# Kernel optimization log

Hardware: AMD Instinct MI355X
Metric: run time of the kernel (lower is better)

## Reference

```python
import jax, jax.numpy as jnp
import numpy as np
from jax import ops

N, E, F_IN, H, M, KC, B, C_OUT = 100000, 1600000, 128, 128, 150000, 60000, 64, 10
BN_EPS = 1e-5

def setup_inputs() -> dict:
    key = jax.random.key(0)
    ks = jax.random.split(key, 16)
    s = 0.05
    x = jax.random.normal(ks[0], (N, F_IN), jnp.float32)
    edge_index = jax.random.randint(ks[1], (2, E), 0, N)
    weights = jax.random.uniform(ks[2], (E,), jnp.float32)
    # sorted batch vector covering all B graphs
    batch = (jnp.arange(N) * B) // N
    # cover assignments: every cluster gets at least one node (arange prefix)
    cover_nodes = jax.random.randint(ks[3], (M,), 0, N)
    cover_clusters = jnp.concatenate([jnp.arange(KC), jax.random.randint(ks[4], (M - KC,), 0, KC)])
    cluster_batch = (jnp.arange(KC) * B) // KC
    out_dim = 4 * H  # 2 * num_layers * hidden, readout=True
    return {
        'x': x, 'edge_index': edge_index, 'weights': weights, 'batch': batch,
        'cover_nodes': cover_nodes, 'cover_clusters': cover_clusters, 'cluster_batch': cluster_batch,
        'W_in': jax.random.normal(ks[5], (F_IN, H), jnp.float32) * s,
        'b_in': jnp.zeros((H,), jnp.float32),
        'W_blk': jax.random.normal(ks[6], (2 * H, H), jnp.float32) * s,
        'b_blk': jnp.zeros((H,), jnp.float32),
        'bn_gamma': jnp.ones((out_dim,), jnp.float32),
        'bn_beta': jnp.zeros((out_dim,), jnp.float32),
        'bn_mean': jnp.zeros((out_dim,), jnp.float32),
        'bn_var': jnp.ones((out_dim,), jnp.float32),
        'W1': jax.random.normal(ks[7], (out_dim, H), jnp.float32) * s,
        'b1': jnp.zeros((H,), jnp.float32),
        'W2': jax.random.normal(ks[8], (H, C_OUT), jnp.float32) * s,
        'b2': jnp.zeros((C_OUT,), jnp.float32),
    }

def _gcn(x, src, dst, w, n, W, b):
    # PyG GCNConv: out = D^-1/2 (A + I) D^-1/2 (x W) + b, weighted degrees incl. self loop of 1
    deg = ops.segment_sum(w, dst, num_segments=n) + 1.0
    dinv = jax.lax.rsqrt(deg)
    xw = x @ W
    msg = (w * dinv[src] * dinv[dst])[:, None] * xw[src]          # [E,H]
    agg = ops.segment_sum(msg, dst, num_segments=n) + (dinv * dinv)[:, None] * xw
    return agg + b

def reference(x, edge_index, weights, batch, cover_nodes, cover_clusters, cluster_batch,
              W_in, b_in, W_blk, b_blk, bn_gamma, bn_beta, bn_mean, bn_var, W1, b1, W2, b2):
    src, dst = edge_index[0], edge_index[1]

    # conv_in + relu
    h = jax.nn.relu(_gcn(x, src, dst, weights, N, W_in, b_in))     # [N,H]

    counts = ops.segment_sum(jnp.ones((N,), jnp.float32), batch, num_segments=B)
    xs = [ops.segment_sum(h, batch, num_segments=B),               # global_add_pool
          ops.segment_max(h, batch, num_segments=B)]               # global_max_pool

    # --- pool_graphs: cover_pool_node (add & max) ---
    x_add = ops.segment_sum(h[cover_nodes], cover_clusters, num_segments=KC)
    x_max = ops.segment_max(h[cover_nodes], cover_clusters, num_segments=KC)
    xp = jnp.concatenate([x_add, x_max], axis=1)                   # [KC, 2H]

    # --- pooled GCN, matrix-free A' = C^T A C (cover_pool_edge, pool='add') ---
    def aprime(z):  # z: [KC, d]
        zn = ops.segment_sum(z[cover_clusters], cover_nodes, num_segments=N)   # C z
        ye = ops.segment_sum(weights[:, None] * zn[src], dst, num_segments=N)  # A (C z)
        return ops.segment_sum(ye[cover_nodes], cover_clusters, num_segments=KC)  # C^T ...

    degp = aprime(jnp.ones((KC, 1), jnp.float32))[:, 0] + 1.0      # weighted degree of A'+I
    dinv = jax.lax.rsqrt(degp)
    xw = xp @ W_blk                                                # [KC,H]
    xws = dinv[:, None] * xw
    hp = jax.nn.relu(dinv[:, None] * (aprime(xws) + xws) + b_blk)  # [KC,H]

    ccounts = ops.segment_sum(jnp.ones((KC,), jnp.float32), cluster_batch, num_segments=B)
    xs.append(ops.segment_sum(hp, cluster_batch, num_segments=B) / ccounts[:, None])  # mean pool
    xs.append(ops.segment_max(hp, cluster_batch, num_segments=B))

    z = jnp.concatenate(xs, axis=1)                                # [B, 4H]
    z = (z - bn_mean) * jax.lax.rsqrt(bn_var + BN_EPS) * bn_gamma + bn_beta  # BN (eval)
    z = jax.nn.relu(z @ W1 + b1)                                   # dropout=identity (eval)
    z = z @ W2 + b2
    return jax.nn.softmax(z, axis=-1)
```

## Files before the change

### kernel.cpp

```cpp
#include <hip/hip_runtime.h>


#define H 128
#define TILE_AGG 2048
#define GRID_AGG 784

typedef __attribute__((ext_vector_type(4))) float f32x4;
typedef __attribute__((ext_vector_type(8))) short bf16x8;

__device__ __forceinline__ void atomAddF(float* p, float v) {
    unsafeAtomicAdd(p, v);
}
__device__ __forceinline__ void atomMaxPos(float* p, float v) {
    atomicMax(reinterpret_cast<int*>(p), __float_as_int(v));
}

__device__ __forceinline__ unsigned int bfr(float f) {
    unsigned int u = __float_as_uint(f);
    return (u + 0x7fffu + ((u >> 16) & 1u)) >> 16;
}
__device__ __forceinline__ unsigned int pk2(float lo, float hi) {
    return bfr(lo) | (bfr(hi) << 16);
}
__device__ __forceinline__ float unlo(unsigned int v) { return __uint_as_float(v << 16); }
__device__ __forceinline__ float unhi(unsigned int v) { return __uint_as_float(v & 0xffff0000u); }

__global__ void count_pairs(const int* __restrict__ a, const int* __restrict__ b,
                            int* __restrict__ ca, int* __restrict__ cb, int M) {
    int i = blockIdx.x * blockDim.x + threadIdx.x;
    if (i < M) {
        atomicAdd(&ca[__builtin_nontemporal_load(a + i)], 1);
        atomicAdd(&cb[__builtin_nontemporal_load(b + i)], 1);
    }
}

__global__ __launch_bounds__(256) void scan_partial(const int* __restrict__ c,
                                                    int* __restrict__ part, int m) {
    __shared__ int red[4];
    int base = blockIdx.x * 1024, t = threadIdx.x;
    int s = 0;
    for (int j = t; j < 1024; j += 256) { int i = base + j; if (i < m) s += c[i]; }
    for (int o = 32; o; o >>= 1) s += __shfl_down(s, o, 64);
    if ((t & 63) == 0) red[t >> 6] = s;
    __syncthreads();
    if (t == 0) part[blockIdx.x] = red[0] + red[1] + red[2] + red[3];
}
__global__ void scan_spine(int* part, int G) {
    if (threadIdx.x == 0) {
        int acc = 0;
        for (int i = 0; i < G; ++i) { int v = part[i]; part[i] = acc; acc += v; }
    }
}
__global__ __launch_bounds__(256) void scan_apply(int* __restrict__ c,
                                                  const int* __restrict__ part, int m) {
    __shared__ int wsum[4];
    int base = blockIdx.x * 1024, t = threadIdx.x;
    int i0 = base + t * 4;
    int v0 = 0, v1 = 0, v2 = 0, v3 = 0;
    if (i0     < m) v0 = c[i0];
    if (i0 + 1 < m) v1 = c[i0 + 1];
    if (i0 + 2 < m) v2 = c[i0 + 2];
    if (i0 + 3 < m) v3 = c[i0 + 3];
    int ts = v0 + v1 + v2 + v3;
    int lane = t & 63, w = t >> 6;
    int sc = ts;
    for (int o = 1; o < 64; o <<= 1) { int u = __shfl_up(sc, o, 64); if (lane >= o) sc += u; }
    if (lane == 63) wsum[w] = sc;
    __syncthreads();
    int off = part[blockIdx.x];
    for (int k = 0; k < w; ++k) off += wsum[k];
    int ex = off + sc - ts;
    if (i0     < m) c[i0]     = ex;
    if (i0 + 1 < m) c[i0 + 1] = ex + v0;
    if (i0 + 2 < m) c[i0 + 2] = ex + v0 + v1;
    if (i0 + 3 < m) c[i0 + 3] = ex + v0 + v1 + v2;
}

__global__ void fill_pairs(const int* __restrict__ key, const int* __restrict__ val,
                           int* __restrict__ offs, int* __restrict__ slots, int M) {
    int i = blockIdx.x * blockDim.x + threadIdx.x;
    int p0 = i * 2, p1 = p0 + 1;
    if (p0 >= M) return;
    int k0 = __builtin_nontemporal_load(key + p0);
    int v0 = __builtin_nontemporal_load(val + p0);
    bool has1 = p1 < M;
    int k1 = k0, v1 = 0;
    if (has1) {
        k1 = __builtin_nontemporal_load(key + p1);
        v1 = __builtin_nontemporal_load(val + p1);
    }
    int q0 = atomicAdd(&offs[k0], 1);
    int q1 = has1 ? atomicAdd(&offs[k1], 1) : 0;
    slots[q0] = v0;
    if (has1) slots[q1] = v1;
}

__global__ __launch_bounds__(256) void hist_coarse(const int* __restrict__ dst,
                                                   int* __restrict__ histc, int E, int Ppad) {
    __shared__ int hb[512];
    for (int i = threadIdx.x; i < 512; i += 256) hb[i] = 0;
    __syncthreads();
    int x = blockIdx.x & 7;
    for (int tile = blockIdx.x; (long)tile * TILE_AGG < E; tile += GRID_AGG) {
        int base = tile * TILE_AGG;
        int lim = min(TILE_AGG, E - base);
        for (int i = threadIdx.x; i < lim; i += 256)
            atomicAdd(&hb[__builtin_nontemporal_load(dst + base + i) >> 8], 1);
    }
    __syncthreads();
    for (int i = threadIdx.x; i < 512; i += 256)
        if (hb[i]) atomicAdd(&histc[x * Ppad + i], hb[i]);
}

__global__ void xpose_c2b(const int* __restrict__ in, int* __restrict__ out, int P, int Ppad) {
    int id = blockIdx.x * blockDim.x + threadIdx.x;
    if (id < P * 8) out[id] = in[(id & 7) * Ppad + (id >> 3)];
}
__global__ void xpose_b2c(const int* __restrict__ in, int* __restrict__ out, int P, int Ppad) {
    int id = blockIdx.x * blockDim.x + threadIdx.x;
    if (id < P * 8) out[(id & 7) * Ppad + (id >> 3)] = in[id];
}

__global__ __launch_bounds__(256) void fill_stage_agg(
    const int* __restrict__ src, const int* __restrict__ dst,
    const float* __restrict__ w, int* __restrict__ cur,
    int2* __restrict__ stg, int E, int Ppad)
{
    __shared__ int cnt[512];
    __shared__ int gbase[512];
    int t = threadIdx.x;
    int x = blockIdx.x & 7;
    for (int tile = blockIdx.x; (long)tile * TILE_AGG < E; tile += GRID_AGG) {
        int base = tile * TILE_AGG;
        int lim = min(TILE_AGG, E - base);
        for (int i = t; i < 512; i += 256) cnt[i] = 0;
        __syncthreads();
        for (int i = t; i < lim; i += 256)
            atomicAdd(&cnt[__builtin_nontemporal_load(dst + base + i) >> 8], 1);
        __syncthreads();
        for (int b = t; b < 512; b += 256) {
            int c = cnt[b];
            if (c) gbase[b] = atomicAdd(&cur[x * Ppad + b], c);
        }
        __syncthreads();
        for (int i = t; i < 512; i += 256) cnt[i] = 0;
        __syncthreads();
        for (int i = t; i < lim; i += 256) {
            int d  = __builtin_nontemporal_load(dst + base + i);
            int s  = __builtin_nontemporal_load(src + base + i);
            float wv = __builtin_nontemporal_load(w + base + i);
            int b = d >> 8;
            int r = atomicAdd(&cnt[b], 1);
            stg[gbase[b] + r] = make_int2(s | ((d & 255) << 20), __float_as_int(wv));
        }
        __syncthreads();
    }
}

__global__ __launch_bounds__(256) void fill_compact(
    const int* __restrict__ curscan, const int2* __restrict__ stg,
    int2* __restrict__ epack, int* __restrict__ ieoffs, int E, int N, int P)
{
    __shared__ int cnt[256];
    __shared__ int wsum[4];
    int b = blockIdx.x, t = threadIdx.x;
    int gs = curscan[b * 8];
    int ge = (b == P - 1) ? E : curscan[(b + 1) * 8];
    cnt[t] = 0;
    __syncthreads();
    for (int i = gs + t; i < ge; i += 256)
        atomicAdd(&cnt[(stg[i].x >> 20) & 255], 1);
    __syncthreads();
    int v = cnt[t];
    int lane = t & 63, wv_ = t >> 6;
    int sc = v;
    for (int o = 1; o < 64; o <<= 1) { int u = __shfl_up(sc, o, 64); if (lane >= o) sc += u; }
    if (lane == 63) wsum[wv_] = sc;
    __syncthreads();
    int off = 0;
    for (int k = 0; k < wv_; ++k) off += wsum[k];
    int excl = off + sc - v;
    int node = b * 256 + t;
    if (node < N) ieoffs[node] = gs + excl + v;
    cnt[t] = excl;
    __syncthreads();
    for (int i = gs + t; i < ge; i += 256) {
        int2 pv = stg[i];
        int pos = atomicAdd(&cnt[(pv.x >> 20) & 255], 1);
        epack[gs + pos] = make_int2(pv.x & 0xFFFFF, pv.y);
    }
}

__global__ void node_scalars(const int* __restrict__ eoffs, const int* __restrict__ epack,
                             const int* __restrict__ qoffs,
                             float* __restrict__ dinv, float* __restrict__ ye1, int N) {
    int n = blockIdx.x * blockDim.x + threadIdx.x;
    if (n >= N) return;
    int b = n ? eoffs[n - 1] : 0, e = eoffs[n];
    float dg = 0.f, y = 0.f;
    for (int i = b; i < e; ++i) {
        int2 pk = ((const int2*)epack)[i];
        float w = __int_as_float(pk.y);
        dg += w;
        int zc = qoffs[pk.x] - (pk.x ? qoffs[pk.x - 1] : 0);
        y += w * (float)zc;
    }
    dinv[n] = rsqrtf(dg + 1.0f);
    ye1[n] = y;
}
__global__ void cluster_dinvp(const int* __restrict__ poffs, const int* __restrict__ pslots,
                              const float* __restrict__ ye1, float* __restrict__ dinvp, int KC) {
    int c = blockIdx.x * blockDim.x + threadIdx.x;
    if (c >= KC) return;
    int b = c ? poffs[c - 1] : 0, e = poffs[c];
    float s = 0.f;
    for (int i = b; i < e; ++i) s += ye1[pslots[i]];
    dinvp[c] = rsqrtf(s + 1.0f);
}

template <int KSTEPS>
__global__ void prepack_w(const float* __restrict__ W, uint4* __restrict__ wp) {
    int idx = blockIdx.x * blockDim.x + threadIdx.x;
    if (idx >= 8 * KSTEPS * 64) return;
    int l = idx & 63;
    int f = idx >> 6;
    int kb = f % KSTEPS, ct = f / KSTEPS;
    int col = ct * 16 + (l & 15);
    int k0 = kb * 32 + (l >> 4) * 8;
    uint4 u;
    u.x = pk2(W[(k0 + 0) * 128 + col], W[(k0 + 1) * 128 + col]);
    u.y = pk2(W[(k0 + 2) * 128 + col], W[(k0 + 3) * 128 + col]);
    u.z = pk2(W[(k0 + 4) * 128 + col], W[(k0 + 5) * 128 + col]);
    u.w = pk2(W[(k0 + 6) * 128 + col], W[(k0 + 7) * 128 + col]);
    wp[idx] = u;
}

template <int KSTEPS>
__global__ __launch_bounds__(256) void gemm_mfma(
    const float* __restrict__ XA,
    const uint4* __restrict__ wpack, const float* __restrict__ rowscale,
    unsigned short* __restrict__ outb, int nrows)
{
    __shared__ uint4 Wl[8 * KSTEPS * 64];
    int t = threadIdx.x;
    for (int i = t; i < 8 * KSTEPS * 64; i += 256) Wl[i] = wpack[i];
    __syncthreads();

    int l = t & 63, wv = t >> 6;
    int row0 = blockIdx.x * 64 + wv * 16;
    int rr = row0 + (l & 15);
    long rc = (rr < nrows ? rr : nrows - 1);
    int kq = (l >> 4) * 8;

    f32x4 acc[8];
#pragma unroll
    for (int ct = 0; ct < 8; ++ct) acc[ct] = (f32x4)0.f;

#pragma unroll
    for (int kb = 0; kb < KSTEPS; ++kb) {
        const float* p = XA + rc * 128 + kb * 32 + kq;
        float4 a0 = ((const float4*)p)[0];
        float4 a1 = ((const float4*)p)[1];
        union { uint4 u; bf16x8 v; } af;
        af.u.x = pk2(a0.x, a0.y); af.u.y = pk2(a0.z, a0.w);
        af.u.z = pk2(a1.x, a1.y); af.u.w = pk2(a1.z, a1.w);
#pragma unroll
        for (int ct = 0; ct < 8; ++ct) {
            union { uint4 u; bf16x8 v; } bf;
            bf.u = Wl[(ct * KSTEPS + kb) * 64 + l];
            acc[ct] = __builtin_amdgcn_mfma_f32_16x16x32_bf16(af.v, bf.v, acc[ct], 0, 0, 0);
        }
    }

    int rbase = row0 + (l >> 4) * 4;
    float sc[4];
#pragma unroll
    for (int g = 0; g < 4; ++g)
        sc[g] = rowscale ? (rbase + g < nrows ? rowscale[rbase + g] : 1.f) : 1.f;
#pragma unroll
    for (int ct = 0; ct < 8; ++ct) {
        int col = ct * 16 + (l & 15);
#pragma unroll
        for (int g = 0; g < 4; ++g) {
            int r = rbase + g;
            if (r < nrows)
                outb[(long)r * 128 + col] = (unsigned short)bfr(acc[ct][g] * sc[g]);
        }
    }
}

__global__ __launch_bounds__(256) void gemm_mfma_bfA(
    const uint4* __restrict__ XA, const uint4* __restrict__ XB,
    const uint4* __restrict__ wpack, const float* __restrict__ rowscale,
    unsigned short* __restrict__ outb, int nrows)
{
    __shared__ uint4 Wl[8 * 8 * 64];
    int t = threadIdx.x;
    for (int i = t; i < 4096; i += 256) Wl[i] = wpack[i];
    __syncthreads();

    int l = t & 63, wv = t >> 6;
    int row0 = blockIdx.x * 64 + wv * 16;
    int rr = row0 + (l & 15);
    long rc = (rr < nrows ? rr : nrows - 1);
    int kq8 = (l >> 4);

    f32x4 acc[8];
#pragma unroll
    for (int ct = 0; ct < 8; ++ct) acc[ct] = (f32x4)0.f;

#pragma unroll
    for (int kb = 0; kb < 8; ++kb) {
        const uint4* s = (kb >= 4) ? XB : XA;
        union { uint4 u; bf16x8 v; } af;
        af.u = s[rc * 16 + (kb & 3) * 4 + kq8];
#pragma unroll
        for (int ct = 0; ct < 8; ++ct) {
            union { uint4 u; bf16x8 v; } bf;
            bf.u = Wl[(ct * 8 + kb) * 64 + l];
            acc[ct] = __builtin_amdgcn_mfma_f32_16x16x32_bf16(af.v, bf.v, acc[ct], 0, 0, 0);
        }
    }

    int rbase = row0 + (l >> 4) * 4;
    float sc[4];
#pragma unroll
    for (int g = 0; g < 4; ++g)
        sc[g] = rowscale ? (rbase + g < nrows ? rowscale[rbase + g] : 1.f) : 1.f;
#pragma unroll
    for (int ct = 0; ct < 8; ++ct) {
        int col = ct * 16 + (l & 15);
#pragma unroll
        for (int g = 0; g < 4; ++g) {
            int r = rbase + g;
            if (r < nrows)
                outb[(long)r * 128 + col] = (unsigned short)bfr(acc[ct][g] * sc[g]);
        }
    }
}

__global__ __launch_bounds__(256) void gcn1_gather(
    const int* __restrict__ eoffs, const int* __restrict__ epack,
    const float* __restrict__ dinv, const unsigned int* __restrict__ xwb,
    const float* __restrict__ bin, unsigned int* __restrict__ hb, int N)
{
    int n = blockIdx.x * 4 + (threadIdx.x >> 6);
    if (n >= N) return;
    int lane = threadIdx.x & 63;
    int cl = lane & 31, half = lane >> 5;
    int b = n ? eoffs[n - 1] : 0, e = eoffs[n];
    const uint2* X = (const uint2*)xwb;
    float4 acc = make_float4(0.f, 0.f, 0.f, 0.f);
    for (int i = b; i < e; i += 64) {
        int cnt = min(64, e - i);
        int s_l = 0; float sc_l = 0.f;
        if (lane < cnt) {
            int2 pk = ((const int2*)epack)[i + lane];
            s_l = pk.x;
            sc_l = __int_as_float(pk.y) * dinv[pk.x];
        }
        int steps = (cnt + 1) >> 1;
#pragma unroll 2
        for (int j = 0; j < steps; ++j) {
            int idx = 2 * j + half;
            int s = __shfl(s_l, idx, 64);
            float sc = __shfl(sc_l, idx, 64);
            uint2 v = X[(long)s * 32 + cl];
            acc.x += sc * unlo(v.x); acc.y += sc * unhi(v.x);
            acc.z += sc * unlo(v.y); acc.w += sc * unhi(v.y);
        }
    }
    acc.x += __shfl_xor(acc.x, 32, 64);
    acc.y += __shfl_xor(acc.y, 32, 64);
    acc.z += __shfl_xor(acc.z, 32, 64);
    acc.w += __shfl_xor(acc.w, 32, 64);
    if (half == 0) {
        float dd = dinv[n];
        uint2 sv = X[(long)n * 32 + cl];
        float4 bb = ((const float4*)bin)[cl];
        float ox = fmaxf(dd * (acc.x + dd * unlo(sv.x)) + bb.x, 0.f);
        float oy = fmaxf(dd * (acc.y + dd * unhi(sv.x)) + bb.y, 0.f);
        float oz = fmaxf(dd * (acc.z + dd * unlo(sv.y)) + bb.z, 0.f);
        float ow = fmaxf(dd * (acc.w + dd * unhi(sv.y)) + bb.w, 0.f);
        ((uint2*)hb)[(long)n * 32 + cl] = make_uint2(pk2(ox, oy), pk2(oz, ow));
    }
}

__global__ __launch_bounds__(256) void edge_gather_plain(
    const int* __restrict__ eoffs, const int* __restrict__ epack,
    const unsigned int* __restrict__ Xb, unsigned int* __restrict__ Outb, int N)
{
    int n = blockIdx.x * 4 + (threadIdx.x >> 6);
    if (n >= N) return;
    int lane = threadIdx.x & 63;
    int cl = lane & 31, half = lane >> 5;
    int b = n ? eoffs[n - 1] : 0, e = eoffs[n];
    const uint2* X = (const uint2*)Xb;
    float4 acc = make_float4(0.f, 0.f, 0.f, 0.f);
    for (int i = b; i < e; i += 64) {
        int cnt = min(64, e - i);
        int s_l = 0; float sc_l = 0.f;
        if (lane < cnt) {
            int2 pk = ((const int2*)epack)[i + lane];
            s_l = pk.x; sc_l = __int_as_float(pk.y);
        }
        int steps = (cnt + 1) >> 1;
#pragma unroll 2
        for (int j = 0; j < steps; ++j) {
            int idx = 2 * j + half;
            int s = __shfl(s_l, idx, 64);
            float sc = __shfl(sc_l, idx, 64);
            uint2 v = X[(long)s * 32 + cl];
            acc.x += sc * unlo(v.x); acc.y += sc * unhi(v.x);
            acc.z += sc * unlo(v.y); acc.w += sc * unhi(v.y);
        }
    }
    acc.x += __shfl_xor(acc.x, 32, 64);
    acc.y += __shfl_xor(acc.y, 32, 64);
    acc.z += __shfl_xor(acc.z, 32, 64);
    acc.w += __shfl_xor(acc.w, 32, 64);
    if (half == 0)
        ((uint2*)Outb)[(long)n * 32 + cl] = make_uint2(pk2(acc.x, acc.y), pk2(acc.z, acc.w));
}

__global__ __launch_bounds__(256) void cover_pool(
    const int* __restrict__ poffs, const int* __restrict__ pslots,
    const unsigned int* __restrict__ hb, unsigned int* __restrict__ xadd,
    unsigned int* __restrict__ xmax, int KC)
{
    int c = blockIdx.x * 8 + (threadIdx.x >> 5);
    if (c >= KC) return;
    int cl = threadIdx.x & 31;
    int b = c ? poffs[c - 1] : 0, e = poffs[c];
    const uint2* Hx = (const uint2*)hb;
    float4 s = make_float4(0.f, 0.f, 0.f, 0.f), m = s;
#pragma unroll 2
    for (int i = b; i < e; ++i) {
        uint2 v = Hx[(long)pslots[i] * 32 + cl];
        float vx = unlo(v.x), vy = unhi(v.x), vz = unlo(v.y), vw = unhi(v.y);
        s.x += vx; s.y += vy; s.z += vz; s.w += vw;
        m.x = fmaxf(m.x, vx); m.y = fmaxf(m.y, vy);
        m.z = fmaxf(m.z, vz); m.w = fmaxf(m.w, vw);
    }
    ((uint2*)xadd)[(long)c * 32 + cl] = make_uint2(pk2(s.x, s.y), pk2(s.z, s.w));
    ((uint2*)xmax)[(long)c * 32 + cl] = make_uint2(pk2(m.x, m.y), pk2(m.z, m.w));
}

__global__ __launch_bounds__(256) void zn_gather(
    const int* __restrict__ qoffs, const int* __restrict__ qslots,
    const unsigned int* __restrict__ xwsb, unsigned int* __restrict__ znb, int N)
{
    int n = blockIdx.x * 8 + (threadIdx.x >> 5);
    if (n >= N) return;
    int cl = threadIdx.x & 31;
    int b = n ? qoffs[n - 1] : 0, e = qoffs[n];
    const uint2* X = (const uint2*)xwsb;
    float4 a = make_float4(0.f, 0.f, 0.f, 0.f);
#pragma unroll 2
    for (int i = b; i < e; ++i) {
        int c = qslots[i];
        uint2 v = X[(long)c * 32 + cl];
        a.x += unlo(v.x); a.y += unhi(v.x);
        a.z += unlo(v.y); a.w += unhi(v.y);
    }
    ((uint2*)znb)[(long)n * 32 + cl] = make_uint2(pk2(a.x, a.y), pk2(a.z, a.w));
}

__global__ __launch_bounds__(256) void aphp_gather(
    const int* __restrict__ poffs, const int* __restrict__ pslots,
    const unsigned int* __restrict__ yeb, const unsigned int* __restrict__ xwsb,
    const float* __restrict__ dinvp, const float* __restrict__ bblk,
    unsigned int* __restrict__ hpb, int KC)
{
    int c = blockIdx.x * 8 + (threadIdx.x >> 5);
    if (c >= KC) return;
    int cl = threadIdx.x & 31;
    int b = c ? poffs[c - 1] : 0, e = poffs[c];
    const uint2* Y = (const uint2*)yeb;
    float4 a = make_float4(0.f, 0.f, 0.f, 0.f);
#pragma unroll 2
    for (int i = b; i < e; ++i) {
        uint2 v = Y[(long)pslots[i] * 32 + cl];
        a.x += unlo(v.x); a.y += unhi(v.x);
        a.z += unlo(v.y); a.w += unhi(v.y);
    }
    float d = dinvp[c];
    uint2 xv = ((const uint2*)xwsb)[(long)c * 32 + cl];
    float4 bb = ((const float4*)bblk)[cl];
    float ox = fmaxf(d * (a.x + unlo(xv.x)) + bb.x, 0.f);
    float oy = fmaxf(d * (a.y + unhi(xv.x)) + bb.y, 0.f);
    float oz = fmaxf(d * (a.z + unlo(xv.y)) + bb.z, 0.f);
    float ow = fmaxf(d * (a.w + unhi(xv.y)) + bb.w, 0.f);
    ((uint2*)hpb)[(long)c * 32 + cl] = make_uint2(pk2(ox, oy), pk2(oz, ow));
}

__global__ __launch_bounds__(128) void seg_pool_bf(
    const unsigned short* __restrict__ X, const int* __restrict__ seg,
    float* __restrict__ Z, int n, int sumoff, int maxoff)
{
    int j = threadIdx.x;
    long beg = (long)blockIdx.x * n / gridDim.x;
    long end = (long)(blockIdx.x + 1) * n / gridDim.x;
    if (beg >= end) return;
    int curb = seg[beg];
    float s = 0.f, mx = 0.f;
    for (long i = beg; i < end; ++i) {
        int b = seg[i];
        if (b != curb) {
            atomAddF(&Z[(long)curb * 512 + sumoff + j], s);
            atomMaxPos(&Z[(long)curb * 512 + maxoff + j], mx);
            s = 0.f; mx = 0.f; curb = b;
        }
        float v = __uint_as_float((unsigned int)X[i * (long)H + j] << 16);
        s += v; mx = fmaxf(mx, v);
    }
    atomAddF(&Z[(long)curb * 512 + sumoff + j], s);
    atomMaxPos(&Z[(long)curb * 512 + maxoff + j], mx);
}

__global__ void hist64(const int* __restrict__ seg, float* __restrict__ cc, int n) {
    __shared__ int hc[128];
    if (threadIdx.x < 128) hc[threadIdx.x] = 0;
    __syncthreads();
    for (int i = blockIdx.x * blockDim.x + threadIdx.x; i < n; i += gridDim.x * blockDim.x)
        atomicAdd(&hc[seg[i]], 1);
    __syncthreads();
    if (threadIdx.x < 128 && hc[threadIdx.x] != 0)
        atomAddF(&cc[threadIdx.x], (float)hc[threadIdx.x]);
}

__global__ __launch_bounds__(128) void head_kernel(
    const float* __restrict__ z, const float* __restrict__ cc,
    const float* __restrict__ gamma, const float* __restrict__ beta,
    const float* __restrict__ bmean, const float* __restrict__ bvar,
    const float* __restrict__ W1, const float* __restrict__ b1,
    const float* __restrict__ W2, const float* __restrict__ b2,
    float* __restrict__ out)
{
    __shared__ float zb[512];
    __shared__ float z1[128];
    __shared__ float lg[10];
    __shared__ float red[2];
    int b = blockIdx.x, t = threadIdx.x;
    float ccb = cc[b];
    for (int k = t; k < 512; k += 128) {
        float v = z[(long)b * 512 + k];
        if (k >= 256 && k < 384) v /= ccb;
        v = (v - bmean[k]) * rsqrtf(bvar[k] + 1e-5f) * gamma[k] + beta[k];
        zb[k] = v;
    }
    __syncthreads();
    float acc = b1[t];
    for (int k = 0; k < 512; ++k) acc += zb[k] * W1[k * 128 + t];
    z1[t] = fmaxf(acc, 0.f);
    __syncthreads();
    if (t < 10) {
        float a = b2[t];
        for (int k = 0; k < 128; ++k) a += z1[k] * W2[k * 10 + t];
        lg[t] = a;
    }
    __syncthreads();
    if (t == 0) {
        float m = lg[0];
        for (int i = 1; i < 10; ++i) m = fmaxf(m, lg[i]);
        float s = 0.f;
        for (int i = 0; i < 10; ++i) s += expf(lg[i] - m);
        red[0] = m; red[1] = s;
    }
    __syncthreads();
    if (t < 10) out[(long)b * 10 + t] = expf(lg[t] - red[0]) / red[1];
}

static void scan_ex(int* buf, int m, int* part, hipStream_t s) {
    int G = (m + 1023) / 1024;
    scan_partial<<<G, 256, 0, s>>>(buf, part, m);
    scan_spine<<<1, 64, 0, s>>>(part, G);
    scan_apply<<<G, 256, 0, s>>>(buf, part, m);
}

extern "C" void kernel_launch(void* const* d_in, const int* in_sizes, int n_in,
                              void* d_out, int out_size, void* d_ws, size_t ws_size,
                              hipStream_t stream)
{
    const float* x      = (const float*)d_in[0];
    const int*   ei     = (const int*)  d_in[1];
    const float* wts    = (const float*)d_in[2];
    const int*   batch  = (const int*)  d_in[3];
    const int*   cnodes = (const int*)  d_in[4];
    const int*   cclus  = (const int*)  d_in[5];
    const int*   cbatch = (const int*)  d_in[6];
    const float* Win    = (const float*)d_in[7];
    const float* bin    = (const float*)d_in[8];
    const float* Wblk   = (const float*)d_in[9];
    const float* bblk   = (const float*)d_in[10];
    const float* gma    = (const float*)d_in[11];
    const float* bta    = (const float*)d_in[12];
    const float* bmean  = (const float*)d_in[13];
    const float* bvar   = (const float*)d_in[14];
    const float* W1     = (const float*)d_in[15];
    const float* b1     = (const float*)d_in[16];
    const float* W2     = (const float*)d_in[17];
    const float* b2     = (const float*)d_in[18];
    float* out = (float*)d_out;

    const int N  = in_sizes[0] / H;
    const int E  = in_sizes[1] / 2;
    const int M  = in_sizes[4];
    const int KC = in_sizes[6];
    const int Bq = out_size / 10;
    const int P  = (N + 255) >> 8;
    const int Ppad = (P + 15) & ~15;

    const int* src = ei;
    const int* dst = ei + E;

    const long NH = (long)N * H;
    const long KH = (long)KC * H;

    float* ws     = (float*)d_ws;
    uint4* wpackN = (uint4*)ws;
    uint4* wpackK = wpackN + 2048;
    unsigned int* Abf = (unsigned int*)(wpackK + 4096);
    unsigned int* Hbf = Abf + NH / 2;
    unsigned int* Cbf = Hbf + NH / 2;
    unsigned int* Fadd= Cbf + KH / 2;
    unsigned int* Fmax= Fadd + KH / 2;
    float* dinv = (float*)(Fmax + KH / 2);
    float* ye1  = dinv + N;
    float* dinvp= ye1 + N;
    float* z    = dinvp + KC;
    float* cc   = z + (long)Bq * 512;
    int* ieoffs = (int*)(cc + Bq);
    int* ipoffs = ieoffs + N;
    int* iqoffs = ipoffs + KC;
    int* epack  = iqoffs + N;
    int* pslots = epack + 2L * E;
    int* qslots = pslots + M;
    int* spart  = qslots + M;
    int* curscan= spart + 2048;
    int* histc  = curscan + P * 8;
    int* curw   = histc + 8 * Ppad;
    int2* estg  = (int2*)(curw + 8 * Ppad);

    hipMemsetAsync(histc, 0, 8 * Ppad * sizeof(int), stream);
    hist_coarse<<<GRID_AGG, 256, 0, stream>>>(dst, histc, E, Ppad);
    xpose_c2b<<<(P * 8 + 255) / 256, 256, 0, stream>>>(histc, curscan, P, Ppad);
    scan_ex(curscan, P * 8, spart, stream);
    xpose_b2c<<<(P * 8 + 255) / 256, 256, 0, stream>>>(curscan, curw, P, Ppad);
    fill_stage_agg<<<GRID_AGG, 256, 0, stream>>>(src, dst, wts, curw, estg, E, Ppad);
    fill_compact<<<P, 256, 0, stream>>>(curscan, estg, (int2*)epack, ieoffs, E, N, P);

    hipMemsetAsync(ipoffs, 0, ((long)KC + N) * sizeof(int), stream);
    count_pairs<<<(M + 255) / 256, 256, 0, stream>>>(cclus, cnodes, ipoffs, iqoffs, M);
    scan_ex(ipoffs, KC, spart, stream);
    scan_ex(iqoffs, N, spart, stream);
    fill_pairs<<<(M / 2 + 256) / 256, 256, 0, stream>>>(cclus, cnodes, ipoffs, pslots, M);
    fill_pairs<<<(M / 2 + 256) / 256, 256, 0, stream>>>(cnodes, cclus, iqoffs, qslots, M);

    prepack_w<4><<<8, 256, 0, stream>>>(Win, wpackN);
    prepack_w<8><<<16, 256, 0, stream>>>(Wblk, wpackK);

    node_scalars<<<(N + 255) / 256, 256, 0, stream>>>(ieoffs, epack, iqoffs, dinv, ye1, N);
    cluster_dinvp<<<(KC + 255) / 256, 256, 0, stream>>>(ipoffs, pslots, ye1, dinvp, KC);

    gemm_mfma<4><<<(N + 63) / 64, 256, 0, stream>>>(x, wpackN, nullptr,
                                                    (unsigned short*)Abf, N);
    gcn1_gather<<<(N + 3) / 4, 256, 0, stream>>>(ieoffs, epack, dinv, Abf, bin, Hbf, N);

    hipMemsetAsync(z, 0, ((long)Bq * 512 + Bq) * sizeof(float), stream);
    cover_pool<<<(KC + 7) / 8, 256, 0, stream>>>(ipoffs, pslots, Hbf, Fadd, Fmax, KC);
    seg_pool_bf<<<1024, 128, 0, stream>>>((const unsigned short*)Hbf, batch, z, N, 0, 128);
    hist64<<<256, 256, 0, stream>>>(cbatch, cc, KC);

    gemm_mfma_bfA<<<(KC + 63) / 64, 256, 0, stream>>>((const uint4*)Fadd, (const uint4*)Fmax,
                                                      wpackK, dinvp,
                                                      (unsigned short*)Cbf, KC);

    zn_gather<<<(N + 7) / 8, 256, 0, stream>>>(iqoffs, qslots, Cbf, Abf, N);
    edge_gather_plain<<<(N + 3) / 4, 256, 0, stream>>>(ieoffs, epack, Abf, Hbf, N);
    aphp_gather<<<(KC + 7) / 8, 256, 0, stream>>>(ipoffs, pslots, Hbf, Cbf, dinvp, bblk, Fadd, KC);

    seg_pool_bf<<<512, 128, 0, stream>>>((const unsigned short*)Fadd, cbatch, z, KC, 256, 384);
    head_kernel<<<Bq, 128, 0, stream>>>(z, cc, gma, bta, bmean, bvar, W1, b1, W2, b2, out);
}
```

Baseline: 495.4 us.

## Widen gather kernels to 16-byte loads and merge small scan kernels

All bf16 row gather kernels (gcn1, edge, cover_pool, zn, aphp) now load a 128-wide row as 16 uint4 per lane group instead of 32 uint2, so each wave processes four neighbors per step and reduces across groups with shuffles. The transpose-scan-transpose sequence for bucket offsets is replaced by a single one-block scan kernel that writes both layouts. fill_compact runs with 1024-thread blocks, and node_scalars reads a precomputed per-node cover count instead of differencing offsets. The intent is fewer memory transactions and fewer launches, at the cost of more registers and a longer cross-group reduction.

```diff
diff --git a/kernel.cpp b/kernel.cpp
--- a/kernel.cpp
+++ b/kernel.cpp
@@ -95,6 +95,11 @@
     if (has1) slots[q1] = v1;
 }
 
+__global__ void qcnt_kernel(const int* __restrict__ qoffs, int* __restrict__ qcnt, int N) {
+    int n = blockIdx.x * blockDim.x + threadIdx.x;
+    if (n < N) qcnt[n] = qoffs[n] - (n ? qoffs[n - 1] : 0);
+}
+
 __global__ __launch_bounds__(256) void hist_coarse(const int* __restrict__ dst,
                                                    int* __restrict__ histc, int E, int Ppad) {
     __shared__ int hb[512];
@@ -112,13 +117,38 @@
         if (hb[i]) atomicAdd(&histc[x * Ppad + i], hb[i]);
 }
 
-__global__ void xpose_c2b(const int* __restrict__ in, int* __restrict__ out, int P, int Ppad) {
-    int id = blockIdx.x * blockDim.x + threadIdx.x;
-    if (id < P * 8) out[id] = in[(id & 7) * Ppad + (id >> 3)];
-}
-__global__ void xpose_b2c(const int* __restrict__ in, int* __restrict__ out, int P, int Ppad) {
-    int id = blockIdx.x * blockDim.x + threadIdx.x;
-    if (id < P * 8) out[(id & 7) * Ppad + (id >> 3)] = in[id];
+__global__ __launch_bounds__(1024) void scan_small(
+    const int* __restrict__ histc, int* __restrict__ curscan,
+    int* __restrict__ curw, int P, int Ppad)
+{
+    __shared__ int wtot[16];
+    int t = threadIdx.x;
+    int m = P * 8;
+    int i0 = t * 4;
+    int v[4];
+#pragma unroll
+    for (int k = 0; k < 4; ++k) {
+        int id = i0 + k;
+        v[k] = (id < m) ? histc[(id & 7) * Ppad + (id >> 3)] : 0;
+    }
+    int ts = v[0] + v[1] + v[2] + v[3];
+    int lane = t & 63, w = t >> 6;
+    int sc = ts;
+    for (int o = 1; o < 64; o <<= 1) { int u = __shfl_up(sc, o, 64); if (lane >= o) sc += u; }
+    if (lane == 63) wtot[w] = sc;
+    __syncthreads();
+    int off = 0;
+    for (int k = 0; k < w; ++k) off += wtot[k];
+    int ex = off + sc - ts;
+#pragma unroll
+    for (int k = 0; k < 4; ++k) {
+        int id = i0 + k;
+        if (id < m) {
+            curscan[id] = ex;
+            curw[(id & 7) * Ppad + (id >> 3)] = ex;
+        }
+        ex += v[k];
+    }
 }
 
 __global__ __launch_bounds__(256) void fill_stage_agg(
@@ -157,7 +187,7 @@
     }
 }
 
-__global__ __launch_bounds__(256) void fill_compact(
+__global__ __launch_bounds__(1024) void fill_compact(
     const int* __restrict__ curscan, const int2* __restrict__ stg,
     int2* __restrict__ epack, int* __restrict__ ieoffs, int E, int N, int P)
 {
@@ -166,25 +196,30 @@
     int b = blockIdx.x, t = threadIdx.x;
     int gs = curscan[b * 8];
     int ge = (b == P - 1) ? E : curscan[(b + 1) * 8];
-    cnt[t] = 0;
-    __syncthreads();
-    for (int i = gs + t; i < ge; i += 256)
+    if (t < 256) cnt[t] = 0;
+    __syncthreads();
+    for (int i = gs + t; i < ge; i += 1024)
         atomicAdd(&cnt[(stg[i].x >> 20) & 255], 1);
     __syncthreads();
-    int v = cnt[t];
-    int lane = t & 63, wv_ = t >> 6;
-    int sc = v;
-    for (int o = 1; o < 64; o <<= 1) { int u = __shfl_up(sc, o, 64); if (lane >= o) sc += u; }
-    if (lane == 63) wsum[wv_] = sc;
-    __syncthreads();
-    int off = 0;
-    for (int k = 0; k < wv_; ++k) off += wsum[k];
-    int excl = off + sc - v;
-    int node = b * 256 + t;
-    if (node < N) ieoffs[node] = gs + excl + v;
-    cnt[t] = excl;
-    __syncthreads();
-    for (int i = gs + t; i < ge; i += 256) {
+    int v = 0, sc = 0;
+    if (t < 256) {
+        v = cnt[t];
+        int lane = t & 63;
+        sc = v;
+        for (int o = 1; o < 64; o <<= 1) { int u = __shfl_up(sc, o, 64); if (lane >= o) sc += u; }
+        if (lane == 63) wsum[t >> 6] = sc;
+    }
+    __syncthreads();
+    if (t < 256) {
+        int off = 0;
+        for (int k = 0; k < (t >> 6); ++k) off += wsum[k];
+        int excl = off + sc - v;
+        int node = b * 256 + t;
+        if (node < N) ieoffs[node] = gs + excl + v;
+        cnt[t] = excl;
+    }
+    __syncthreads();
+    for (int i = gs + t; i < ge; i += 1024) {
         int2 pv = stg[i];
         int pos = atomicAdd(&cnt[(pv.x >> 20) & 255], 1);
         epack[gs + pos] = make_int2(pv.x & 0xFFFFF, pv.y);
@@ -192,7 +227,7 @@
 }
 
 __global__ void node_scalars(const int* __restrict__ eoffs, const int* __restrict__ epack,
-                             const int* __restrict__ qoffs,
+                             const int* __restrict__ qcnt,
                              float* __restrict__ dinv, float* __restrict__ ye1, int N) {
     int n = blockIdx.x * blockDim.x + threadIdx.x;
     if (n >= N) return;
@@ -202,8 +237,7 @@
         int2 pk = ((const int2*)epack)[i];
         float w = __int_as_float(pk.y);
         dg += w;
-        int zc = qoffs[pk.x] - (pk.x ? qoffs[pk.x - 1] : 0);
-        y += w * (float)zc;
+        y += w * (float)qcnt[pk.x];
     }
     dinv[n] = rsqrtf(dg + 1.0f);
     ye1[n] = y;
@@ -339,18 +373,18 @@
     }
 }
 
+
 __global__ __launch_bounds__(256) void gcn1_gather(
     const int* __restrict__ eoffs, const int* __restrict__ epack,
-    const float* __restrict__ dinv, const unsigned int* __restrict__ xwb,
-    const float* __restrict__ bin, unsigned int* __restrict__ hb, int N)
+    const float* __restrict__ dinv, const uint4* __restrict__ X4,
+    const float* __restrict__ bin, uint4* __restrict__ H4, int N)
 {
     int n = blockIdx.x * 4 + (threadIdx.x >> 6);
     if (n >= N) return;
     int lane = threadIdx.x & 63;
-    int cl = lane & 31, half = lane >> 5;
+    int ql = lane & 15, grp = lane >> 4;
     int b = n ? eoffs[n - 1] : 0, e = eoffs[n];
-    const uint2* X = (const uint2*)xwb;
-    float4 acc = make_float4(0.f, 0.f, 0.f, 0.f);
+    float4 a0 = make_float4(0.f, 0.f, 0.f, 0.f), a1 = a0;
     for (int i = b; i < e; i += 64) {
         int cnt = min(64, e - i);
         int s_l = 0; float sc_l = 0.f;
@@ -359,44 +393,54 @@
             s_l = pk.x;
             sc_l = __int_as_float(pk.y) * dinv[pk.x];
         }
-        int steps = (cnt + 1) >> 1;
+        int steps = (cnt + 3) >> 2;
 #pragma unroll 2
         for (int j = 0; j < steps; ++j) {
-            int idx = 2 * j + half;
+            int idx = 4 * j + grp;
             int s = __shfl(s_l, idx, 64);
             float sc = __shfl(sc_l, idx, 64);
-            uint2 v = X[(long)s * 32 + cl];
-            acc.x += sc * unlo(v.x); acc.y += sc * unhi(v.x);
-            acc.z += sc * unlo(v.y); acc.w += sc * unhi(v.y);
-        }
-    }
-    acc.x += __shfl_xor(acc.x, 32, 64);
-    acc.y += __shfl_xor(acc.y, 32, 64);
-    acc.z += __shfl_xor(acc.z, 32, 64);
-    acc.w += __shfl_xor(acc.w, 32, 64);
-    if (half == 0) {
+            uint4 v = X4[(long)s * 16 + ql];
+            a0.x += sc * unlo(v.x); a0.y += sc * unhi(v.x);
+            a0.z += sc * unlo(v.y); a0.w += sc * unhi(v.y);
+            a1.x += sc * unlo(v.z); a1.y += sc * unhi(v.z);
+            a1.z += sc * unlo(v.w); a1.w += sc * unhi(v.w);
+        }
+    }
+#pragma unroll
+    for (int o = 16; o <= 32; o <<= 1) {
+        a0.x += __shfl_xor(a0.x, o, 64); a0.y += __shfl_xor(a0.y, o, 64);
+        a0.z += __shfl_xor(a0.z, o, 64); a0.w += __shfl_xor(a0.w, o, 64);
+        a1.x += __shfl_xor(a1.x, o, 64); a1.y += __shfl_xor(a1.y, o, 64);
+        a1.z += __shfl_xor(a1.z, o, 64); a1.w += __shfl_xor(a1.w, o, 64);
+    }
+    if (grp == 0) {
         float dd = dinv[n];
-        uint2 sv = X[(long)n * 32 + cl];
-        float4 bb = ((const float4*)bin)[cl];
-        float ox = fmaxf(dd * (acc.x + dd * unlo(sv.x)) + bb.x, 0.f);
-        float oy = fmaxf(dd * (acc.y + dd * unhi(sv.x)) + bb.y, 0.f);
-        float oz = fmaxf(dd * (acc.z + dd * unlo(sv.y)) + bb.z, 0.f);
-        float ow = fmaxf(dd * (acc.w + dd * unhi(sv.y)) + bb.w, 0.f);
-        ((uint2*)hb)[(long)n * 32 + cl] = make_uint2(pk2(ox, oy), pk2(oz, ow));
+        uint4 sv = X4[(long)n * 16 + ql];
+        float4 b0 = ((const float4*)bin)[ql * 2];
+        float4 b1 = ((const float4*)bin)[ql * 2 + 1];
+        float o0 = fmaxf(dd * (a0.x + dd * unlo(sv.x)) + b0.x, 0.f);
+        float o1 = fmaxf(dd * (a0.y + dd * unhi(sv.x)) + b0.y, 0.f);
+        float o2 = fmaxf(dd * (a0.z + dd * unlo(sv.y)) + b0.z, 0.f);
+        float o3 = fmaxf(dd * (a0.w + dd * unhi(sv.y)) + b0.w, 0.f);
+        float o4 = fmaxf(dd * (a1.x + dd * unlo(sv.z)) + b1.x, 0.f);
+        float o5 = fmaxf(dd * (a1.y + dd * unhi(sv.z)) + b1.y, 0.f);
+        float o6 = fmaxf(dd * (a1.z + dd * unlo(sv.w)) + b1.z, 0.f);
+        float o7 = fmaxf(dd * (a1.w + dd * unhi(sv.w)) + b1.w, 0.f);
+        H4[(long)n * 16 + ql] = make_uint4(pk2(o0, o1), pk2(o2, o3),
+                                           pk2(o4, o5), pk2(o6, o7));
     }
 }
 
 __global__ __launch_bounds__(256) void edge_gather_plain(
     const int* __restrict__ eoffs, const int* __restrict__ epack,
-    const unsigned int* __restrict__ Xb, unsigned int* __restrict__ Outb, int N)
+    const uint4* __restrict__ X4, uint4* __restrict__ Out4, int N)
 {
     int n = blockIdx.x * 4 + (threadIdx.x >> 6);
     if (n >= N) return;
     int lane = threadIdx.x & 63;
-    int cl = lane & 31, half = lane >> 5;
+    int ql = lane & 15, grp = lane >> 4;
     int b = n ? eoffs[n - 1] : 0, e = eoffs[n];
-    const uint2* X = (const uint2*)Xb;
-    float4 acc = make_float4(0.f, 0.f, 0.f, 0.f);
+    float4 a0 = make_float4(0.f, 0.f, 0.f, 0.f), a1 = a0;
     for (int i = b; i < e; i += 64) {
         int cnt = min(64, e - i);
         int s_l = 0; float sc_l = 0.f;
@@ -404,94 +448,109 @@
             int2 pk = ((const int2*)epack)[i + lane];
             s_l = pk.x; sc_l = __int_as_float(pk.y);
         }
-        int steps = (cnt + 1) >> 1;
+        int steps = (cnt + 3) >> 2;
 #pragma unroll 2
         for (int j = 0; j < steps; ++j) {
-            int idx = 2 * j + half;
+            int idx = 4 * j + grp;
             int s = __shfl(s_l, idx, 64);
             float sc = __shfl(sc_l, idx, 64);
-            uint2 v = X[(long)s * 32 + cl];
-            acc.x += sc * unlo(v.x); acc.y += sc * unhi(v.x);
-            acc.z += sc * unlo(v.y); acc.w += sc * unhi(v.y);
-        }
-    }
-    acc.x += __shfl_xor(acc.x, 32, 64);
-    acc.y += __shfl_xor(acc.y, 32, 64);
-    acc.z += __shfl_xor(acc.z, 32, 64);
-    acc.w += __shfl_xor(acc.w, 32, 64);
-    if (half == 0)
-        ((uint2*)Outb)[(long)n * 32 + cl] = make_uint2(pk2(acc.x, acc.y), pk2(acc.z, acc.w));
+            uint4 v = X4[(long)s * 16 + ql];
+            a0.x += sc * unlo(v.x); a0.y += sc * unhi(v.x);
+            a0.z += sc * unlo(v.y); a0.w += sc * unhi(v.y);
+            a1.x += sc * unlo(v.z); a1.y += sc * unhi(v.z);
+            a1.z += sc * unlo(v.w); a1.w += sc * unhi(v.w);
+        }
+    }
+#pragma unroll
+    for (int o = 16; o <= 32; o <<= 1) {
+        a0.x += __shfl_xor(a0.x, o, 64); a0.y += __shfl_xor(a0.y, o, 64);
+        a0.z += __shfl_xor(a0.z, o, 64); a0.w += __shfl_xor(a0.w, o, 64);
+        a1.x += __shfl_xor(a1.x, o, 64); a1.y += __shfl_xor(a1.y, o, 64);
+        a1.z += __shfl_xor(a1.z, o, 64); a1.w += __shfl_xor(a1.w, o, 64);
+    }
+    if (grp == 0)
+        Out4[(long)n * 16 + ql] = make_uint4(pk2(a0.x, a0.y), pk2(a0.z, a0.w),
+                                             pk2(a1.x, a1.y), pk2(a1.z, a1.w));
 }
 
 __global__ __launch_bounds__(256) void cover_pool(
     const int* __restrict__ poffs, const int* __restrict__ pslots,
-    const unsigned int* __restrict__ hb, unsigned int* __restrict__ xadd,
-    unsigned int* __restrict__ xmax, int KC)
-{
-    int c = blockIdx.x * 8 + (threadIdx.x >> 5);
+    const uint4* __restrict__ H4, uint4* __restrict__ xadd,
+    uint4* __restrict__ xmax, int KC)
+{
+    int c = blockIdx.x * 16 + (threadIdx.x >> 4);
     if (c >= KC) return;
-    int cl = threadIdx.x & 31;
+    int ql = threadIdx.x & 15;
     int b = c ? poffs[c - 1] : 0, e = poffs[c];
-    const uint2* Hx = (const uint2*)hb;
-    float4 s = make_float4(0.f, 0.f, 0.f, 0.f), m = s;
+    float4 s0 = make_float4(0.f, 0.f, 0.f, 0.f), s1 = s0, m0 = s0, m1 = s0;
 #pragma unroll 2
     for (int i = b; i < e; ++i) {
-        uint2 v = Hx[(long)pslots[i] * 32 + cl];
-        float vx = unlo(v.x), vy = unhi(v.x), vz = unlo(v.y), vw = unhi(v.y);
-        s.x += vx; s.y += vy; s.z += vz; s.w += vw;
-        m.x = fmaxf(m.x, vx); m.y = fmaxf(m.y, vy);
-        m.z = fmaxf(m.z, vz); m.w = fmaxf(m.w, vw);
-    }
-    ((uint2*)xadd)[(long)c * 32 + cl] = make_uint2(pk2(s.x, s.y), pk2(s.z, s.w));
-    ((uint2*)xmax)[(long)c * 32 + cl] = make_uint2(pk2(m.x, m.y), pk2(m.z, m.w));
+        uint4 v = H4[(long)pslots[i] * 16 + ql];
+        float e0 = unlo(v.x), e1 = unhi(v.x), e2 = unlo(v.y), e3 = unhi(v.y);
+        float e4 = unlo(v.z), e5 = unhi(v.z), e6 = unlo(v.w), e7 = unhi(v.w);
+        s0.x += e0; s0.y += e1; s0.z += e2; s0.w += e3;
+        s1.x += e4; s1.y += e5; s1.z += e6; s1.w += e7;
+        m0.x = fmaxf(m0.x, e0); m0.y = fmaxf(m0.y, e1);
+        m0.z = fmaxf(m0.z, e2); m0.w = fmaxf(m0.w, e3);
+        m1.x = fmaxf(m1.x, e4); m1.y = fmaxf(m1.y, e5);
+        m1.z = fmaxf(m1.z, e6); m1.w = fmaxf(m1.w, e7);
+    }
+    xadd[(long)c * 16 + ql] = make_uint4(pk2(s0.x, s0.y), pk2(s0.z, s0.w),
+                                         pk2(s1.x, s1.y), pk2(s1.z, s1.w));
+    xmax[(long)c * 16 + ql] = make_uint4(pk2(m0.x, m0.y), pk2(m0.z, m0.w),
+                                         pk2(m1.x, m1.y), pk2(m1.z, m1.w));
 }
 
 __global__ __launch_bounds__(256) void zn_gather(
     const int* __restrict__ qoffs, const int* __restrict__ qslots,
-    const unsigned int* __restrict__ xwsb, unsigned int* __restrict__ znb, int N)
-{
-    int n = blockIdx.x * 8 + (threadIdx.x >> 5);
+    const uint4* __restrict__ X4, uint4* __restrict__ Z4, int N)
+{
+    int n = blockIdx.x * 16 + (threadIdx.x >> 4);
     if (n >= N) return;
-    int cl = threadIdx.x & 31;
+    int ql = threadIdx.x & 15;
     int b = n ? qoffs[n - 1] : 0, e = qoffs[n];
-    const uint2* X = (const uint2*)xwsb;
-    float4 a = make_float4(0.f, 0.f, 0.f, 0.f);
+    float4 a0 = make_float4(0.f, 0.f, 0.f, 0.f), a1 = a0;
 #pragma unroll 2
     for (int i = b; i < e; ++i) {
-        int c = qslots[i];
-        uint2 v = X[(long)c * 32 + cl];
-        a.x += unlo(v.x); a.y += unhi(v.x);
-        a.z += unlo(v.y); a.w += unhi(v.y);
-    }
-    ((uint2*)znb)[(long)n * 32 + cl] = make_uint2(pk2(a.x, a.y), pk2(a.z, a.w));
+        uint4 v = X4[(long)qslots[i] * 16 + ql];
+        a0.x += unlo(v.x); a0.y += unhi(v.x); a0.z += unlo(v.y); a0.w += unhi(v.y);
+        a1.x += unlo(v.z); a1.y += unhi(v.z); a1.z += unlo(v.w); a1.w += unhi(v.w);
+    }
+    Z4[(long)n * 16 + ql] = make_uint4(pk2(a0.x, a0.y), pk2(a0.z, a0.w),
+                                       pk2(a1.x, a1.y), pk2(a1.z, a1.w));
 }
 
 __global__ __launch_bounds__(256) void aphp_gather(
     const int* __restrict__ poffs, const int* __restrict__ pslots,
-    const unsigned int* __restrict__ yeb, const unsigned int* __restrict__ xwsb,
+    const uint4* __restrict__ Y4, const uint4* __restrict__ xws4,
     const float* __restrict__ dinvp, const float* __restrict__ bblk,
-    unsigned int* __restrict__ hpb, int KC)
-{
-    int c = blockIdx.x * 8 + (threadIdx.x >> 5);
+    uint4* __restrict__ hp4, int KC)
+{
+    int c = blockIdx.x * 16 + (threadIdx.x >> 4);
     if (c >= KC) return;
-    int cl = threadIdx.x & 31;
+    int ql = threadIdx.x & 15;
     int b = c ? poffs[c - 1] : 0, e = poffs[c];
-    const uint2* Y = (const uint2*)yeb;
-    float4 a = make_float4(0.f, 0.f, 0.f, 0.f);
+    float4 a0 = make_float4(0.f, 0.f, 0.f, 0.f), a1 = a0;
 #pragma unroll 2
     for (int i = b; i < e; ++i) {
-        uint2 v = Y[(long)pslots[i] * 32 + cl];
-        a.x += unlo(v.x); a.y += unhi(v.x);
-        a.z += unlo(v.y); a.w += unhi(v.y);
+        uint4 v = Y4[(long)pslots[i] * 16 + ql];
+        a0.x += unlo(v.x); a0.y += unhi(v.x); a0.z += unlo(v.y); a0.w += unhi(v.y);
+        a1.x += unlo(v.z); a1.y += unhi(v.z); a1.z += unlo(v.w); a1.w += unhi(v.w);
     }
     float d = dinvp[c];
-    uint2 xv = ((const uint2*)xwsb)[(long)c * 32 + cl];
-    float4 bb = ((const float4*)bblk)[cl];
-    float ox = fmaxf(d * (a.x + unlo(xv.x)) + bb.x, 0.f);
-    float oy = fmaxf(d * (a.y + unhi(xv.x)) + bb.y, 0.f);
-    float oz = fmaxf(d * (a.z + unlo(xv.y)) + bb.z, 0.f);
-    float ow = fmaxf(d * (a.w + unhi(xv.y)) + bb.w, 0.f);
-    ((uint2*)hpb)[(long)c * 32 + cl] = make_uint2(pk2(ox, oy), pk2(oz, ow));
+    uint4 xv = xws4[(long)c * 16 + ql];
+    float4 b0 = ((const float4*)bblk)[ql * 2];
+    float4 b1 = ((const float4*)bblk)[ql * 2 + 1];
+    float o0 = fmaxf(d * (a0.x + unlo(xv.x)) + b0.x, 0.f);
+    float o1 = fmaxf(d * (a0.y + unhi(xv.x)) + b0.y, 0.f);
+    float o2 = fmaxf(d * (a0.z + unlo(xv.y)) + b0.z, 0.f);
+    float o3 = fmaxf(d * (a0.w + unhi(xv.y)) + b0.w, 0.f);
+    float o4 = fmaxf(d * (a1.x + unlo(xv.z)) + b1.x, 0.f);
+    float o5 = fmaxf(d * (a1.y + unhi(xv.z)) + b1.y, 0.f);
+    float o6 = fmaxf(d * (a1.z + unlo(xv.w)) + b1.z, 0.f);
+    float o7 = fmaxf(d * (a1.w + unhi(xv.w)) + b1.w, 0.f);
+    hp4[(long)c * 16 + ql] = make_uint4(pk2(o0, o1), pk2(o2, o3),
+                                        pk2(o4, o5), pk2(o6, o7));
 }
 
 __global__ __launch_bounds__(128) void seg_pool_bf(
@@ -640,15 +699,14 @@
     int* curscan= spart + 2048;
     int* histc  = curscan + P * 8;
     int* curw   = histc + 8 * Ppad;
-    int2* estg  = (int2*)(curw + 8 * Ppad);
+    int* qcnt   = curw + 8 * Ppad;
+    int2* estg  = (int2*)(qcnt + N);
 
     hipMemsetAsync(histc, 0, 8 * Ppad * sizeof(int), stream);
     hist_coarse<<<GRID_AGG, 256, 0, stream>>>(dst, histc, E, Ppad);
-    xpose_c2b<<<(P * 8 + 255) / 256, 256, 0, stream>>>(histc, curscan, P, Ppad);
-    scan_ex(curscan, P * 8, spart, stream);
-    xpose_b2c<<<(P * 8 + 255) / 256, 256, 0, stream>>>(curscan, curw, P, Ppad);
+    scan_small<<<1, 1024, 0, stream>>>(histc, curscan, curw, P, Ppad);
     fill_stage_agg<<<GRID_AGG, 256, 0, stream>>>(src, dst, wts, curw, estg, E, Ppad);
-    fill_compact<<<P, 256, 0, stream>>>(curscan, estg, (int2*)epack, ieoffs, E, N, P);
+    fill_compact<<<P, 1024, 0, stream>>>(curscan, estg, (int2*)epack, ieoffs, E, N, P);
 
     hipMemsetAsync(ipoffs, 0, ((long)KC + N) * sizeof(int), stream);
     count_pairs<<<(M + 255) / 256, 256, 0, stream>>>(cclus, cnodes, ipoffs, iqoffs, M);
@@ -656,19 +714,23 @@
     scan_ex(iqoffs, N, spart, stream);
     fill_pairs<<<(M / 2 + 256) / 256, 256, 0, stream>>>(cclus, cnodes, ipoffs, pslots, M);
     fill_pairs<<<(M / 2 + 256) / 256, 256, 0, stream>>>(cnodes, cclus, iqoffs, qslots, M);
+    qcnt_kernel<<<(N + 255) / 256, 256, 0, stream>>>(iqoffs, qcnt, N);
 
     prepack_w<4><<<8, 256, 0, stream>>>(Win, wpackN);
     prepack_w<8><<<16, 256, 0, stream>>>(Wblk, wpackK);
 
-    node_scalars<<<(N + 255) / 256, 256, 0, stream>>>(ieoffs, epack, iqoffs, dinv, ye1, N);
+    node_scalars<<<(N + 255) / 256, 256, 0, stream>>>(ieoffs, epack, qcnt, dinv, ye1, N);
     cluster_dinvp<<<(KC + 255) / 256, 256, 0, stream>>>(ipoffs, pslots, ye1, dinvp, KC);
 
     gemm_mfma<4><<<(N + 63) / 64, 256, 0, stream>>>(x, wpackN, nullptr,
                                                     (unsigned short*)Abf, N);
-    gcn1_gather<<<(N + 3) / 4, 256, 0, stream>>>(ieoffs, epack, dinv, Abf, bin, Hbf, N);
+    gcn1_gather<<<(N + 3) / 4, 256, 0, stream>>>(ieoffs, epack, dinv,
+                                                 (const uint4*)Abf, bin,
+                                                 (uint4*)Hbf, N);
 
     hipMemsetAsync(z, 0, ((long)Bq * 512 + Bq) * sizeof(float), stream);
-    cover_pool<<<(KC + 7) / 8, 256, 0, stream>>>(ipoffs, pslots, Hbf, Fadd, Fmax, KC);
+    cover_pool<<<(KC + 15) / 16, 256, 0, stream>>>(ipoffs, pslots, (const uint4*)Hbf,
+                                                   (uint4*)Fadd, (uint4*)Fmax, KC);
     seg_pool_bf<<<1024, 128, 0, stream>>>((const unsigned short*)Hbf, batch, z, N, 0, 128);
     hist64<<<256, 256, 0, stream>>>(cbatch, cc, KC);
 
@@ -676,9 +738,14 @@
                                                       wpackK, dinvp,
                                                       (unsigned short*)Cbf, KC);
 
-    zn_gather<<<(N + 7) / 8, 256, 0, stream>>>(iqoffs, qslots, Cbf, Abf, N);
-    edge_gather_plain<<<(N + 3) / 4, 256, 0, stream>>>(ieoffs, epack, Abf, Hbf, N);
-    aphp_gather<<<(KC + 7) / 8, 256, 0, stream>>>(ipoffs, pslots, Hbf, Cbf, dinvp, bblk, Fadd, KC);
+    zn_gather<<<(N + 15) / 16, 256, 0, stream>>>(iqoffs, qslots, (const uint4*)Cbf,
+                                                 (uint4*)Abf, N);
+    edge_gather_plain<<<(N + 3) / 4, 256, 0, stream>>>(ieoffs, epack,
+                                                       (const uint4*)Abf,
+                                                       (uint4*)Hbf, N);
+    aphp_gather<<<(KC + 15) / 16, 256, 0, stream>>>(ipoffs, pslots, (const uint4*)Hbf,
+                                                    (const uint4*)Cbf, dinvp, bblk,
+                                                    (uint4*)Fadd, KC);
 
     seg_pool_bf<<<512, 128, 0, stream>>>((const unsigned short*)Fadd, cbatch, z, KC, 256, 384);
     head_kernel<<<Bq, 128, 0, stream>>>(z, cc, gma, bta, bmean, bvar, W1, b1, W2, b2, out);
```

Measured after the change: 455.3 us. -8.1%, faster.
